# Kernel tuning notes

Hardware: AMD Instinct MI355X
Metric: run time of the kernel (lower is better)

The kernel has to match this reference:

```python
import jax, jax.numpy as jnp
import numpy as np

def setup_inputs() -> dict:
    key = jax.random.key(0)
    ks = jax.random.split(key, 8)
    E, D_IN, D_OUT = 250000, 256, 256
    NUM_CAMS, NUM_POINTS = 500, 100000
    return {
        "edge_features": jax.random.normal(ks[0], (E, D_IN), dtype=jnp.float32),
        "cam_indices": jax.random.randint(ks[1], (E,), 0, NUM_CAMS, dtype=jnp.int64 if jax.config.jax_enable_x64 else jnp.int32),
        "point_indices": jax.random.randint(ks[2], (E,), 0, NUM_POINTS, dtype=jnp.int64 if jax.config.jax_enable_x64 else jnp.int32),
        "num_cams": NUM_CAMS,
        "num_points": NUM_POINTS,
        "W_cam": jax.random.normal(ks[3], (D_OUT, D_IN), dtype=jnp.float32) / np.sqrt(D_IN),
        "W_point": jax.random.normal(ks[4], (D_OUT, D_IN), dtype=jnp.float32) / np.sqrt(D_IN),
        "W_attn": jax.random.normal(ks[5], (1, 2 * D_OUT), dtype=jnp.float32) / np.sqrt(2 * D_OUT),
        "W_final": jax.random.normal(ks[6], (D_OUT, 2 * D_OUT), dtype=jnp.float32) / np.sqrt(2 * D_OUT),
        "b_final": jax.random.normal(ks[7], (D_OUT,), dtype=jnp.float32) * 0.01,
    }

def reference(edge_features, cam_indices, point_indices, num_cams, num_points,
              W_cam, W_point, W_attn, W_final, b_final):
    # scatter-add aggregation per camera / per point node
    cam_agg = jax.ops.segment_sum(edge_features, cam_indices, num_segments=num_cams)      # [C, d_in]
    point_agg = jax.ops.segment_sum(edge_features, point_indices, num_segments=num_points)  # [P, d_in]
    # node projections (torch Linear: y = x @ W.T)
    h_cam = cam_agg @ W_cam.T        # [C, d_out]
    h_point = point_agg @ W_point.T  # [P, d_out]
    # gather back per edge and concat
    concat = jnp.concatenate([h_cam[cam_indices], h_point[point_indices]], axis=1)  # [E, 2*d_out]
    # attention score with GLOBAL softmax over all edges (dim=0)
    e = concat @ W_attn.T                       # [E, 1]
    attn = jax.nn.softmax(e, axis=0)            # [E, 1]
    new_features = (concat @ W_final.T + b_final) * attn  # [E, d_out]
    return jax.nn.relu(new_features)
```

## Files before the change

kernel.cpp:

```cpp
#include <hip/hip_runtime.h>
#include <hip/hip_bf16.h>
#include <math.h>

#define D 256
#define NCAM 500
#define NPT 100000

__global__ void scatter_kernel(const float* __restrict__ ef,
                               const int* __restrict__ ci,
                               const int* __restrict__ pi,
                               float* __restrict__ cam_agg,
                               float* __restrict__ pt_agg, int E) {
    int e = blockIdx.x;
    if (e >= E) return;
    int c = ci[e];
    int p = pi[e];
    int f = threadIdx.x;
    float v = ef[(size_t)e * D + f];
    atomicAdd(&pt_agg[(size_t)p * D + f], v);
    atomicAdd(&cam_agg[(size_t)c * D + f], v);
}

__global__ void combine_weights(const float* __restrict__ Wcam,
                                const float* __restrict__ Wpt,
                                const float* __restrict__ Wattn,
                                const float* __restrict__ Wfin,
                                float* __restrict__ CcamT,
                                float* __restrict__ Cpt,
                                float* __restrict__ vcam,
                                float* __restrict__ vpt) {
    int b = blockIdx.x;
    int i = threadIdx.x;
    if (b < 256) {
        int o = b;
        float acc = 0.f;
        for (int j = 0; j < 256; j++) acc += Wfin[o * 512 + j] * Wcam[j * 256 + i];
        CcamT[i * 256 + o] = acc;
    } else if (b < 512) {
        int o = b - 256;
        float acc = 0.f;
        for (int j = 0; j < 256; j++) acc += Wfin[o * 512 + 256 + j] * Wpt[j * 256 + i];
        Cpt[o * 256 + i] = acc;
    } else if (b == 512) {
        float acc = 0.f;
        for (int j = 0; j < 256; j++) acc += Wattn[j] * Wcam[j * 256 + i];
        vcam[i] = acc;
    } else {
        float acc = 0.f;
        for (int j = 0; j < 256; j++) acc += Wattn[256 + j] * Wpt[j * 256 + i];
        vpt[i] = acc;
    }
}

__global__ void cam_proj(const float* __restrict__ cam_agg,
                         const float* __restrict__ CcamT,
                         const float* __restrict__ vcam,
                         float* __restrict__ gcam,
                         float* __restrict__ acam) {
    __shared__ float row[256];
    __shared__ float red[256];
    int c = blockIdx.x;
    int t = threadIdx.x;
    row[t] = cam_agg[(size_t)c * 256 + t];
    __syncthreads();
    float acc = 0.f;
    for (int i = 0; i < 256; i++) acc += row[i] * CcamT[i * 256 + t];
    gcam[(size_t)c * 256 + t] = acc;
    red[t] = row[t] * vcam[t];
    __syncthreads();
    for (int s = 128; s > 0; s >>= 1) {
        if (t < s) red[t] += red[t + s];
        __syncthreads();
    }
    if (t == 0) acam[c] = red[0];
}

#define BM 64
#define BN 64
#define BK 32
__global__ __launch_bounds__(256) void gemm_pt(const float* __restrict__ A,
                                               const float* __restrict__ Bmat,
                                               float* __restrict__ Cout, int M) {
    __shared__ float As[BK][BM + 4];
    __shared__ float Bs[BK][BN + 4];
    int m0 = blockIdx.x * BM;
    int n0 = blockIdx.y * BN;
    int tid = threadIdx.x;
    int arow = tid >> 2;
    int acol = (tid & 3) * 8;
    int tm = (tid >> 4) << 2;
    int tn = (tid & 15) << 2;
    float acc[4][4] = {};
    for (int k0 = 0; k0 < 256; k0 += BK) {
        const float* aptr = A + (size_t)(m0 + arow) * 256 + k0 + acol;
        float4 av0 = *(const float4*)aptr;
        float4 av1 = *(const float4*)(aptr + 4);
        const float* bptr = Bmat + (size_t)(n0 + arow) * 256 + k0 + acol;
        float4 bv0 = *(const float4*)bptr;
        float4 bv1 = *(const float4*)(bptr + 4);
        As[acol + 0][arow] = av0.x; As[acol + 1][arow] = av0.y;
        As[acol + 2][arow] = av0.z; As[acol + 3][arow] = av0.w;
        As[acol + 4][arow] = av1.x; As[acol + 5][arow] = av1.y;
        As[acol + 6][arow] = av1.z; As[acol + 7][arow] = av1.w;
        Bs[acol + 0][arow] = bv0.x; Bs[acol + 1][arow] = bv0.y;
        Bs[acol + 2][arow] = bv0.z; Bs[acol + 3][arow] = bv0.w;
        Bs[acol + 4][arow] = bv1.x; Bs[acol + 5][arow] = bv1.y;
        Bs[acol + 6][arow] = bv1.z; Bs[acol + 7][arow] = bv1.w;
        __syncthreads();
#pragma unroll
        for (int k = 0; k < BK; k++) {
            float4 a = *(const float4*)&As[k][tm];
            float4 b = *(const float4*)&Bs[k][tn];
            acc[0][0] += a.x * b.x; acc[0][1] += a.x * b.y; acc[0][2] += a.x * b.z; acc[0][3] += a.x * b.w;
            acc[1][0] += a.y * b.x; acc[1][1] += a.y * b.y; acc[1][2] += a.y * b.z; acc[1][3] += a.y * b.w;
            acc[2][0] += a.z * b.x; acc[2][1] += a.z * b.y; acc[2][2] += a.z * b.z; acc[2][3] += a.z * b.w;
            acc[3][0] += a.w * b.x; acc[3][1] += a.w * b.y; acc[3][2] += a.w * b.z; acc[3][3] += a.w * b.w;
        }
        __syncthreads();
    }
#pragma unroll
    for (int i = 0; i < 4; i++) {
        int m = m0 + tm + i;
        if (m < M) {
            float4 v = make_float4(acc[i][0], acc[i][1], acc[i][2], acc[i][3]);
            *(float4*)&Cout[(size_t)m * 256 + n0 + tn] = v;
        }
    }
}

__global__ void apt_kernel(const float* __restrict__ A,
                           const float* __restrict__ vpt,
                           float* __restrict__ apt, int M) {
    __shared__ float vs[256];
    vs[threadIdx.x] = vpt[threadIdx.x];
    __syncthreads();
    int wave = threadIdx.x >> 6;
    int lane = threadIdx.x & 63;
    int row = blockIdx.x * 4 + wave;
    if (row >= M) return;
    const float* a = A + (size_t)row * 256;
    float acc = 0.f;
    for (int i = lane; i < 256; i += 64) acc += a[i] * vs[i];
    for (int off = 32; off > 0; off >>= 1) acc += __shfl_down(acc, off);
    if (lane == 0) apt[row] = acc;
}

__device__ __forceinline__ unsigned float_key(float f) {
    unsigned b = __float_as_uint(f);
    return (b & 0x80000000u) ? ~b : (b | 0x80000000u);
}
__device__ __forceinline__ float key_float(unsigned k) {
    return __uint_as_float((k & 0x80000000u) ? (k & 0x7FFFFFFFu) : ~k);
}

__global__ void e_max_kernel(const int* __restrict__ ci, const int* __restrict__ pi,
                             const float* __restrict__ acam, const float* __restrict__ apt,
                             float* __restrict__ ebuf, unsigned* __restrict__ maxkey, int E) {
    int i = blockIdx.x * 256 + threadIdx.x;
    float e = -INFINITY;
    if (i < E) {
        e = acam[ci[i]] + apt[pi[i]];
        ebuf[i] = e;
    }
    __shared__ float red[256];
    int t = threadIdx.x;
    red[t] = e;
    __syncthreads();
    for (int s = 128; s > 0; s >>= 1) {
        if (t < s) red[t] = fmaxf(red[t], red[t + s]);
        __syncthreads();
    }
    if (t == 0) atomicMax(maxkey, float_key(red[0]));
}

__global__ void sumexp_kernel(float* __restrict__ ebuf,
                              const unsigned* __restrict__ maxkey,
                              float* __restrict__ sumexp, int E) {
    int i = blockIdx.x * 256 + threadIdx.x;
    float mx = key_float(*maxkey);
    float p = 0.f;
    if (i < E) {
        p = expf(ebuf[i] - mx);
        ebuf[i] = p;
    }
    __shared__ float red[256];
    int t = threadIdx.x;
    red[t] = p;
    __syncthreads();
    for (int s = 128; s > 0; s >>= 1) {
        if (t < s) red[t] += red[t + s];
        __syncthreads();
    }
    if (t == 0) atomicAdd(sumexp, red[0]);
}

__global__ void out_kernel(const int* __restrict__ ci, const int* __restrict__ pi,
                           const float* __restrict__ gcam, const float* __restrict__ gpt,
                           const float* __restrict__ bfin, const float* __restrict__ ebuf,
                           const float* __restrict__ sumexp, float* __restrict__ out, int E) {
    int e = blockIdx.x;
    int t = threadIdx.x;
    float scale = ebuf[e] / (*sumexp);
    int c = ci[e];
    int p = pi[e];
    float v = (gcam[(size_t)c * 256 + t] + gpt[(size_t)p * 256 + t] + bfin[t]) * scale;
    out[(size_t)e * 256 + t] = fmaxf(v, 0.f);
}

extern "C" void kernel_launch(void* const* d_in, const int* in_sizes, int n_in,
                              void* d_out, int out_size, void* d_ws, size_t ws_size,
                              hipStream_t stream) {
    const float* ef    = (const float*)d_in[0];
    const int*   ci    = (const int*)d_in[1];
    const int*   pi    = (const int*)d_in[2];
    const float* Wcam  = (const float*)d_in[5];
    const float* Wpt   = (const float*)d_in[6];
    const float* Wattn = (const float*)d_in[7];
    const float* Wfin  = (const float*)d_in[8];
    const float* bfin  = (const float*)d_in[9];
    float* out = (float*)d_out;
    int E = in_sizes[0] / D;

    float* ws = (float*)d_ws;
    float* cam_agg = ws;
    float* pt_agg  = cam_agg + (size_t)NCAM * D;
    float* CcamT   = pt_agg + (size_t)NPT * D;
    float* Cpt     = CcamT + 65536;
    float* vcam    = Cpt + 65536;
    float* vpt     = vcam + 256;
    float* gcam    = vpt + 256;
    float* acam    = gcam + (size_t)NCAM * D;
    float* gpt     = acam + 512;
    float* apt     = gpt + (size_t)NPT * D;
    float* ebuf    = apt + NPT;
    unsigned* maxkey = (unsigned*)(ebuf + E);
    float* sumexp  = (float*)(maxkey + 1);

    hipMemsetAsync(cam_agg, 0, (size_t)(NCAM + NPT) * D * sizeof(float), stream);
    hipMemsetAsync(maxkey, 0, 2 * sizeof(unsigned), stream);

    scatter_kernel<<<E, 256, 0, stream>>>(ef, ci, pi, cam_agg, pt_agg, E);
    combine_weights<<<514, 256, 0, stream>>>(Wcam, Wpt, Wattn, Wfin, CcamT, Cpt, vcam, vpt);
    cam_proj<<<NCAM, 256, 0, stream>>>(cam_agg, CcamT, vcam, gcam, acam);
    dim3 g4((NPT + BM - 1) / BM, 256 / BN);
    gemm_pt<<<g4, 256, 0, stream>>>(pt_agg, Cpt, gpt, NPT);
    apt_kernel<<<(NPT + 3) / 4, 256, 0, stream>>>(pt_agg, vpt, apt, NPT);
    int eb = (E + 255) / 256;
    e_max_kernel<<<eb, 256, 0, stream>>>(ci, pi, acam, apt, ebuf, maxkey, E);
    sumexp_kernel<<<eb, 256, 0, stream>>>(ebuf, maxkey, sumexp, E);
    out_kernel<<<E, 256, 0, stream>>>(ci, pi, gcam, gpt, bfin, ebuf, sumexp, out, E);
}
```

Baseline: 1.158 ms.

## Replace atomic scatter with CSR bucketing and gather-based segment sums

The per-element atomic scatter of edge features into the point and camera aggregates is replaced by a counting sort. A histogram, a single-block scan and a bucketing pass build per-node edge lists, and the segment sums are then computed by gathering rows per node. The point dot product with vpt is fused into the point aggregation kernel, which removes the separate apt pass and the large memset of pt_agg. Camera aggregation uses 8 partial sums per camera combined with atomics, so it no longer needs one atomic per edge element. This adds several small kernels, including a serial single-block scan over 100k counts, and the order within each bucket is nondeterministic, so float summation order can vary between runs.

```diff
diff --git a/kernel.cpp b/kernel.cpp
--- a/kernel.cpp
+++ b/kernel.cpp
@@ -6,19 +6,113 @@
 #define NCAM 500
 #define NPT 100000
 
-__global__ void scatter_kernel(const float* __restrict__ ef,
-                               const int* __restrict__ ci,
-                               const int* __restrict__ pi,
-                               float* __restrict__ cam_agg,
-                               float* __restrict__ pt_agg, int E) {
-    int e = blockIdx.x;
-    if (e >= E) return;
-    int c = ci[e];
-    int p = pi[e];
-    int f = threadIdx.x;
-    float v = ef[(size_t)e * D + f];
-    atomicAdd(&pt_agg[(size_t)p * D + f], v);
-    atomicAdd(&cam_agg[(size_t)c * D + f], v);
+__global__ void hist_kernel(const int* __restrict__ ci, const int* __restrict__ pi,
+                            int* __restrict__ cnt_pt, int* __restrict__ cnt_cam, int E) {
+    int i = blockIdx.x * 256 + threadIdx.x;
+    if (i < E) {
+        atomicAdd(&cnt_pt[pi[i]], 1);
+        atomicAdd(&cnt_cam[ci[i]], 1);
+    }
+}
+
+__global__ __launch_bounds__(1024) void scan_kernel(const int* __restrict__ cnt_pt,
+                                                    const int* __restrict__ cnt_cam,
+                                                    int* __restrict__ off_pt,
+                                                    int* __restrict__ cur_pt,
+                                                    int* __restrict__ off_cam,
+                                                    int* __restrict__ cur_cam) {
+    __shared__ int lds[1024];
+    int t = threadIdx.x;
+    const int CH = (NPT + 1023) / 1024;
+    int b0 = t * CH;
+    int b1 = b0 + CH; if (b1 > NPT) b1 = NPT;
+    int s = 0;
+    for (int i = b0; i < b1; i++) s += cnt_pt[i];
+    lds[t] = s;
+    __syncthreads();
+    for (int off = 1; off < 1024; off <<= 1) {
+        int v = (t >= off) ? lds[t - off] : 0;
+        __syncthreads();
+        lds[t] += v;
+        __syncthreads();
+    }
+    int run = (t == 0) ? 0 : lds[t - 1];
+    for (int i = b0; i < b1; i++) {
+        int c = cnt_pt[i];
+        off_pt[i] = run;
+        cur_pt[i] = run;
+        run += c;
+    }
+    if (t == 1023) off_pt[NPT] = lds[1023];
+    __syncthreads();
+    if (t < 512) lds[t] = (t < NCAM) ? cnt_cam[t] : 0;
+    __syncthreads();
+    for (int off = 1; off < 512; off <<= 1) {
+        int v = 0;
+        if (t < 512 && t >= off) v = lds[t - off];
+        __syncthreads();
+        if (t < 512 && t >= off) lds[t] += v;
+        __syncthreads();
+    }
+    if (t < NCAM) {
+        int ex = (t == 0) ? 0 : lds[t - 1];
+        off_cam[t] = ex;
+        cur_cam[t] = ex;
+    }
+    if (t == NCAM) off_cam[NCAM] = lds[NCAM - 1];
+}
+
+__global__ void bucket_kernel(const int* __restrict__ ci, const int* __restrict__ pi,
+                              int* __restrict__ cur_pt, int* __restrict__ cur_cam,
+                              int* __restrict__ order_pt, int* __restrict__ order_cam,
+                              int E) {
+    int i = blockIdx.x * 256 + threadIdx.x;
+    if (i < E) {
+        int pos = atomicAdd(&cur_pt[pi[i]], 1);
+        order_pt[pos] = i;
+        int pos2 = atomicAdd(&cur_cam[ci[i]], 1);
+        order_cam[pos2] = i;
+    }
+}
+
+__global__ void pt_agg_kernel(const float* __restrict__ ef,
+                              const int* __restrict__ order_pt,
+                              const int* __restrict__ off_pt,
+                              const float* __restrict__ vpt,
+                              float* __restrict__ pt_agg,
+                              float* __restrict__ apt) {
+    int wave = threadIdx.x >> 6;
+    int lane = threadIdx.x & 63;
+    int p = blockIdx.x * 4 + wave;
+    if (p >= NPT) return;
+    int j0 = off_pt[p], j1 = off_pt[p + 1];
+    float4 acc = make_float4(0.f, 0.f, 0.f, 0.f);
+    for (int j = j0; j < j1; j++) {
+        int e = order_pt[j];
+        float4 v = *(const float4*)(ef + (size_t)e * D + lane * 4);
+        acc.x += v.x; acc.y += v.y; acc.z += v.z; acc.w += v.w;
+    }
+    *(float4*)(pt_agg + (size_t)p * D + lane * 4) = acc;
+    float4 vv = *(const float4*)(vpt + lane * 4);
+    float d = acc.x * vv.x + acc.y * vv.y + acc.z * vv.z + acc.w * vv.w;
+    for (int off = 32; off > 0; off >>= 1) d += __shfl_down(d, off);
+    if (lane == 0) apt[p] = d;
+}
+
+__global__ void cam_agg_kernel(const float* __restrict__ ef,
+                               const int* __restrict__ order_cam,
+                               const int* __restrict__ off_cam,
+                               float* __restrict__ cam_agg) {
+    int c = blockIdx.x;
+    int q = blockIdx.y;
+    int t = threadIdx.x;
+    int j0 = off_cam[c], j1 = off_cam[c + 1];
+    float acc = 0.f;
+    for (int j = j0 + q; j < j1; j += 8) {
+        int e = order_cam[j];
+        acc += ef[(size_t)e * D + t];
+    }
+    atomicAdd(&cam_agg[(size_t)c * D + t], acc);
 }
 
 __global__ void combine_weights(const float* __restrict__ Wcam,
@@ -128,23 +222,6 @@
     }
 }
 
-__global__ void apt_kernel(const float* __restrict__ A,
-                           const float* __restrict__ vpt,
-                           float* __restrict__ apt, int M) {
-    __shared__ float vs[256];
-    vs[threadIdx.x] = vpt[threadIdx.x];
-    __syncthreads();
-    int wave = threadIdx.x >> 6;
-    int lane = threadIdx.x & 63;
-    int row = blockIdx.x * 4 + wave;
-    if (row >= M) return;
-    const float* a = A + (size_t)row * 256;
-    float acc = 0.f;
-    for (int i = lane; i < 256; i += 64) acc += a[i] * vs[i];
-    for (int off = 32; off > 0; off >>= 1) acc += __shfl_down(acc, off);
-    if (lane == 0) apt[row] = acc;
-}
-
 __device__ __forceinline__ unsigned float_key(float f) {
     unsigned b = __float_as_uint(f);
     return (b & 0x80000000u) ? ~b : (b | 0x80000000u);
@@ -236,16 +313,30 @@
     unsigned* maxkey = (unsigned*)(ebuf + E);
     float* sumexp  = (float*)(maxkey + 1);
 
-    hipMemsetAsync(cam_agg, 0, (size_t)(NCAM + NPT) * D * sizeof(float), stream);
+    int* ib        = (int*)gpt;
+    int* cnt_pt    = ib;
+    int* cnt_cam   = cnt_pt + NPT;
+    int* off_pt    = cnt_cam + NCAM;
+    int* off_cam   = off_pt + NPT + 1;
+    int* cur_pt    = off_cam + NCAM + 1;
+    int* cur_cam   = cur_pt + NPT;
+    int* order_pt  = cur_cam + NCAM;
+    int* order_cam = order_pt + E;
+
+    hipMemsetAsync(cam_agg, 0, (size_t)NCAM * D * sizeof(float), stream);
     hipMemsetAsync(maxkey, 0, 2 * sizeof(unsigned), stream);
-
-    scatter_kernel<<<E, 256, 0, stream>>>(ef, ci, pi, cam_agg, pt_agg, E);
+    hipMemsetAsync(cnt_pt, 0, (size_t)(NPT + NCAM) * sizeof(int), stream);
+
+    int eb = (E + 255) / 256;
+    hist_kernel<<<eb, 256, 0, stream>>>(ci, pi, cnt_pt, cnt_cam, E);
     combine_weights<<<514, 256, 0, stream>>>(Wcam, Wpt, Wattn, Wfin, CcamT, Cpt, vcam, vpt);
+    scan_kernel<<<1, 1024, 0, stream>>>(cnt_pt, cnt_cam, off_pt, cur_pt, off_cam, cur_cam);
+    bucket_kernel<<<eb, 256, 0, stream>>>(ci, pi, cur_pt, cur_cam, order_pt, order_cam, E);
+    pt_agg_kernel<<<(NPT + 3) / 4, 256, 0, stream>>>(ef, order_pt, off_pt, vpt, pt_agg, apt);
+    cam_agg_kernel<<<dim3(NCAM, 8), 256, 0, stream>>>(ef, order_cam, off_cam, cam_agg);
     cam_proj<<<NCAM, 256, 0, stream>>>(cam_agg, CcamT, vcam, gcam, acam);
     dim3 g4((NPT + BM - 1) / BM, 256 / BN);
     gemm_pt<<<g4, 256, 0, stream>>>(pt_agg, Cpt, gpt, NPT);
-    apt_kernel<<<(NPT + 3) / 4, 256, 0, stream>>>(pt_agg, vpt, apt, NPT);
-    int eb = (E + 255) / 256;
     e_max_kernel<<<eb, 256, 0, stream>>>(ci, pi, acam, apt, ebuf, maxkey, E);
     sumexp_kernel<<<eb, 256, 0, stream>>>(ebuf, maxkey, sumexp, E);
     out_kernel<<<E, 256, 0, stream>>>(ci, pi, gcam, gpt, bfin, ebuf, sumexp, out, E);
```

After: 1.329 ms. +14.8%, slower.
